# Optimization experiments

Hardware: AMD Instinct MI355X
Metric: run time of the kernel (lower is better)

Reference implementation:

```python
import jax, jax.numpy as jnp
import numpy as np

S_MAX = 512   # BERT max positions (module filters spans to <=512)


def setup_inputs() -> dict:
    key = jax.random.key(0)
    k1, k2, k3, k4, k5 = jax.random.split(key, 5)
    B, S, H = 8, 512, 768
    E, M, C = 16, 4, 96
    embedding = jax.random.normal(k1, (B, S, H), dtype=jnp.float32)
    # mean-over-heads last-layer attention rows (row-stochastic-ish positives)
    attention = jax.random.uniform(k2, (B, S, S), dtype=jnp.float32)
    attention = attention / attention.sum(-1, keepdims=True)
    mention_starts = jax.random.randint(k3, (B, E, M), 0, 500, dtype=jnp.int32)
    mention_lengths = jax.random.randint(k4, (B, E, M), 1, 6, dtype=jnp.int32)
    labels = jax.random.randint(k5, (B, E, E, C), 0, 2, dtype=jnp.int32)
    return {"embedding": embedding, "attention": attention,
            "mention_starts": mention_starts, "mention_lengths": mention_lengths,
            "labels": labels}


def reference(embedding, attention, mention_starts, mention_lengths, labels):
    # embedding: [B,S,H] BERT last_hidden_state
    # attention: [B,S,S] last-layer attention averaged over heads
    # mention spans (start, end): tokens start+1 .. end inclusive (per original slicing)
    B, S, H = embedding.shape
    E = mention_starts.shape[1]
    s_idx = jnp.arange(S, dtype=jnp.int32)
    ends = mention_starts + mention_lengths
    # token membership mask per entity: union over its mentions. [B,E,S]
    mask = ((s_idx >= (mention_starts + 1)[..., None]) &
            (s_idx <= ends[..., None])).any(axis=2)
    maskf = mask.astype(embedding.dtype)
    count = jnp.maximum(maskf.sum(-1, keepdims=True), 1.0)  # [B,E,1]
    # context[e] = mean over selected tokens t of attention[t] @ embedding
    att_rows = jnp.einsum('bes,bst->bet', maskf, attention)          # summed attention rows
    context = jnp.einsum('bet,bth->beh', att_rows, embedding) / count  # [B,E,H]
    # doc[e] = logsumexp over selected token embeddings (per hidden dim)
    masked = jnp.where(mask[..., None], embedding[:, None, :, :], -jnp.inf)  # [B,E,S,H]
    doc = jax.scipy.special.logsumexp(masked, axis=2)                # [B,E,H]
    cls = embedding[:, 0]                                            # [B,H]
    # all ordered entity pairs h != t (use_negative=True path)
    hh, tt = np.nonzero(~np.eye(E, dtype=bool))                      # static, P = E*(E-1)
    P = hh.shape[0]
    feat = jnp.stack([
        jnp.broadcast_to(cls[:, None, :], (B, P, H)),
        doc[:, hh],
        doc[:, tt],
        context[:, hh] * context[:, tt],
    ], axis=2)                                                       # [B,P,4,H]
    feature_set = feat.reshape(B * P, 4, H)
    labels_out = labels[:, hh, tt].reshape(B * P, -1)                # [B*P,C]
    return feature_set, labels_out
```

## Files before the change

### kernel.cpp

```cpp
#include <hip/hip_runtime.h>
#include <math.h>

#define Bc 8
#define Sc 512
#define Hc 768
#define Ec 16
#define Mc 4
#define Cc 96
#define Pc 240


__global__ __launch_bounds__(256) void k_mask_att_doc(
    const float* __restrict__ emb, const float* __restrict__ att,
    const int* __restrict__ starts, const int* __restrict__ lens,
    float* __restrict__ att_rows, float* __restrict__ cnt,
    float* __restrict__ docv, float* __restrict__ ctxu)
{
  int be = blockIdx.x;
  int b  = be >> 4;
  int tid = threadIdx.x;

  {
    float* z = ctxu + (size_t)be * Hc;
    z[tid] = 0.f; z[tid + 256] = 0.f; z[tid + 512] = 0.f;
  }

  __shared__ int slist[32];
  __shared__ int n_sh;
  if (tid == 0) n_sh = 0;
  __syncthreads();

  int base = be * Mc;
  int st0 = starts[base+0], st1 = starts[base+1];
  int st2 = starts[base+2], st3 = starts[base+3];
  int en0 = st0 + lens[base+0], en1 = st1 + lens[base+1];
  int en2 = st2 + lens[base+2], en3 = st3 + lens[base+3];

  for (int s = tid; s < Sc; s += 256) {
    bool in = (s > st0 && s <= en0) || (s > st1 && s <= en1) ||
              (s > st2 && s <= en2) || (s > st3 && s <= en3);
    if (in) { int pos = atomicAdd(&n_sh, 1); slist[pos] = s; }
  }
  __syncthreads();
  int n = n_sh;

  float2 a = make_float2(0.f, 0.f);
  for (int i = 0; i < n; ++i) {
    const float2* row2 =
        (const float2*)(att + ((size_t)b * Sc + slist[i]) * Sc);
    float2 v = row2[tid];
    a.x += v.x; a.y += v.y;
  }
  ((float2*)(att_rows + (size_t)be * Sc))[tid] = a;
  if (tid == 0) cnt[be] = (float)n;

  #pragma unroll
  for (int kk = 0; kk < 3; ++kk) {
    int h = tid + kk * 256;
    const float* ecol = emb + (size_t)b * Sc * Hc + h;
    float m = ecol[(size_t)slist[0] * Hc];
    float l = 1.0f;
    for (int i = 1; i < n; ++i) {
      float v  = ecol[(size_t)slist[i] * Hc];
      float nm = fmaxf(m, v);
      l = l * __expf(m - nm) + __expf(v - nm);
      m = nm;
    }
    docv[(size_t)be * Hc + h] = m + __logf(l);
  }
}

__global__ __launch_bounds__(256) void k_context(
    const float* __restrict__ emb, const float* __restrict__ att_rows,
    float* __restrict__ ctxu)
{
  int tchunk = blockIdx.x;
  int hchunk = blockIdx.y;
  int b      = blockIdx.z;
  int tid = threadIdx.x;
  int h  = hchunk * 256 + tid;
  int t0 = tchunk * 64;

  __shared__ float ar[64][20];
  {
    int e = tid >> 4, q = tid & 15;
    const float4* src =
        (const float4*)(att_rows + ((size_t)(b * Ec + e)) * Sc + t0);
    float4 v = src[q];
    ar[q*4+0][e] = v.x;
    ar[q*4+1][e] = v.y;
    ar[q*4+2][e] = v.z;
    ar[q*4+3][e] = v.w;
  }
  __syncthreads();

  float acc[16];
  #pragma unroll
  for (int e = 0; e < 16; ++e) acc[e] = 0.f;

  const float* ecol = emb + ((size_t)b * Sc + t0) * Hc + h;
  #pragma unroll 4
  for (int tt = 0; tt < 64; ++tt) {
    float ev = ecol[(size_t)tt * Hc];
    const float4* arv = (const float4*)&ar[tt][0];
    float4 a0 = arv[0], a1 = arv[1], a2 = arv[2], a3 = arv[3];
    acc[ 0] = fmaf(a0.x, ev, acc[ 0]);
    acc[ 1] = fmaf(a0.y, ev, acc[ 1]);
    acc[ 2] = fmaf(a0.z, ev, acc[ 2]);
    acc[ 3] = fmaf(a0.w, ev, acc[ 3]);
    acc[ 4] = fmaf(a1.x, ev, acc[ 4]);
    acc[ 5] = fmaf(a1.y, ev, acc[ 5]);
    acc[ 6] = fmaf(a1.z, ev, acc[ 6]);
    acc[ 7] = fmaf(a1.w, ev, acc[ 7]);
    acc[ 8] = fmaf(a2.x, ev, acc[ 8]);
    acc[ 9] = fmaf(a2.y, ev, acc[ 9]);
    acc[10] = fmaf(a2.z, ev, acc[10]);
    acc[11] = fmaf(a2.w, ev, acc[11]);
    acc[12] = fmaf(a3.x, ev, acc[12]);
    acc[13] = fmaf(a3.y, ev, acc[13]);
    acc[14] = fmaf(a3.z, ev, acc[14]);
    acc[15] = fmaf(a3.w, ev, acc[15]);
  }

  float* outb = ctxu + (size_t)(b * Ec) * Hc + h;
  #pragma unroll
  for (int e = 0; e < 16; ++e) atomicAdd(outb + (size_t)e * Hc, acc[e]);
}

__global__ __launch_bounds__(192) void k_assemble(
    const float* __restrict__ emb, const int* __restrict__ labels,
    const float* __restrict__ docv, const float* __restrict__ ctxu,
    const float* __restrict__ cnt, float* __restrict__ out)
{
  int r = blockIdx.x;
  int b = r / Pc, p = r % Pc;
  int i = p / 15, k = p % 15;
  int j = k + (k >= i ? 1 : 0);
  int tid = threadIdx.x;

  float ci = 1.0f / cnt[b * Ec + i];
  float cj = 1.0f / cnt[b * Ec + j];

  const float4* cls4 = (const float4*)(emb  + (size_t)b * Sc * Hc);
  const float4* di4  = (const float4*)(docv + (size_t)(b * Ec + i) * Hc);
  const float4* dj4  = (const float4*)(docv + (size_t)(b * Ec + j) * Hc);
  const float4* xi4  = (const float4*)(ctxu + (size_t)(b * Ec + i) * Hc);
  const float4* xj4  = (const float4*)(ctxu + (size_t)(b * Ec + j) * Hc);
  float4* o = (float4*)(out + (size_t)r * 4 * Hc);

  o[      tid] = cls4[tid];
  o[192 + tid] = di4[tid];
  o[384 + tid] = dj4[tid];
  float4 xa = xi4[tid], xb = xj4[tid], c;
  c.x = (xa.x * ci) * (xb.x * cj);
  c.y = (xa.y * ci) * (xb.y * cj);
  c.z = (xa.z * ci) * (xb.z * cj);
  c.w = (xa.w * ci) * (xb.w * cj);
  o[576 + tid] = c;

  if (tid < 24) {
    const int4* l4 =
        (const int4*)(labels + (((size_t)b * Ec + i) * Ec + j) * Cc);
    int4 v = l4[tid];
    float4 f;
    f.x = (float)v.x; f.y = (float)v.y; f.z = (float)v.z; f.w = (float)v.w;
    ((float4*)(out + (size_t)Bc * Pc * 4 * Hc + (size_t)r * Cc))[tid] = f;
  }
}

extern "C" void kernel_launch(void* const* d_in, const int* in_sizes, int n_in,
                              void* d_out, int out_size, void* d_ws, size_t ws_size,
                              hipStream_t stream) {
  const float* emb    = (const float*)d_in[0];
  const float* att    = (const float*)d_in[1];
  const int*   starts = (const int*)d_in[2];
  const int*   lens   = (const int*)d_in[3];
  const int*   labels = (const int*)d_in[4];
  float* out = (float*)d_out;

  float* att_rows = (float*)d_ws;
  float* cnt      = att_rows + (size_t)Bc * Ec * Sc;
  float* docv     = cnt      + (size_t)Bc * Ec;
  float* ctxu     = docv     + (size_t)Bc * Ec * Hc;

  k_mask_att_doc<<<Bc * Ec, 256, 0, stream>>>(emb, att, starts, lens,
                                              att_rows, cnt, docv, ctxu);
  k_context<<<dim3(8, 3, Bc), 256, 0, stream>>>(emb, att_rows, ctxu);
  k_assemble<<<Bc * Pc, 192, 0, stream>>>(emb, labels, docv, ctxu, cnt, out);
}
```

Measured before the change: 98.86 us.

## Fuse three kernels into one cooperative kernel with grid syncs

Merges the mask/attention/doc, context and assemble kernels into a single cooperatively launched kernel of 192 blocks, using grid-wide syncs between phases so that two kernel launches and their gaps go away. The logsumexp becomes a two-pass max-then-sum with four independent accumulators, and the attention-row gather is unrolled by four. Assembly now runs on only 192 blocks that each loop over 10 rows, which lowers parallelism for the output-write phase. Grid syncs add their own cost, and the two-pass logsumexp reads the gathered embeddings twice.

```diff
diff --git a/kernel.cpp b/kernel.cpp
--- a/kernel.cpp
+++ b/kernel.cpp
@@ -1,5 +1,8 @@
 #include <hip/hip_runtime.h>
+#include <hip/hip_cooperative_groups.h>
 #include <math.h>
+
+namespace cg = cooperative_groups;
 
 #define Bc 8
 #define Sc 512
@@ -8,163 +11,187 @@
 #define Mc 4
 #define Cc 96
 #define Pc 240
-
-
-__global__ __launch_bounds__(256) void k_mask_att_doc(
+#define NB 192
+
+
+__global__ __launch_bounds__(256) void k_fused(
     const float* __restrict__ emb, const float* __restrict__ att,
     const int* __restrict__ starts, const int* __restrict__ lens,
+    const int* __restrict__ labels,
     float* __restrict__ att_rows, float* __restrict__ cnt,
-    float* __restrict__ docv, float* __restrict__ ctxu)
+    float* __restrict__ docv, float* __restrict__ ctxu,
+    float* __restrict__ out)
 {
-  int be = blockIdx.x;
-  int b  = be >> 4;
-  int tid = threadIdx.x;
+  cg::grid_group gg = cg::this_grid();
+  const int bid = blockIdx.x;
+  const int tid = threadIdx.x;
+
+  __shared__ int   slist[32];
+  __shared__ int   n_sh;
+  __shared__ float ar[64][20];
+
+  if (bid < Bc * Ec) {
+    const int be = bid, b = be >> 4;
+
+    {
+      float* z = ctxu + (size_t)be * Hc;
+      z[tid] = 0.f; z[tid + 256] = 0.f; z[tid + 512] = 0.f;
+    }
+
+    if (tid == 0) n_sh = 0;
+    __syncthreads();
+    const int base = be * Mc;
+    const int st0 = starts[base+0], st1 = starts[base+1];
+    const int st2 = starts[base+2], st3 = starts[base+3];
+    const int en0 = st0 + lens[base+0], en1 = st1 + lens[base+1];
+    const int en2 = st2 + lens[base+2], en3 = st3 + lens[base+3];
+    for (int s = tid; s < Sc; s += 256) {
+      bool in = (s > st0 && s <= en0) || (s > st1 && s <= en1) ||
+                (s > st2 && s <= en2) || (s > st3 && s <= en3);
+      if (in) { int pos = atomicAdd(&n_sh, 1); slist[pos] = s; }
+    }
+    __syncthreads();
+    const int n = n_sh;
+
+    {
+      const float2* a2 = (const float2*)(att + (size_t)b * Sc * Sc);
+      float2 acc2 = make_float2(0.f, 0.f);
+      int i = 0;
+      for (; i + 4 <= n; i += 4) {
+        float2 v0 = a2[(size_t)slist[i+0] * (Sc/2) + tid];
+        float2 v1 = a2[(size_t)slist[i+1] * (Sc/2) + tid];
+        float2 v2 = a2[(size_t)slist[i+2] * (Sc/2) + tid];
+        float2 v3 = a2[(size_t)slist[i+3] * (Sc/2) + tid];
+        acc2.x += (v0.x + v1.x) + (v2.x + v3.x);
+        acc2.y += (v0.y + v1.y) + (v2.y + v3.y);
+      }
+      for (; i < n; ++i) {
+        float2 v = a2[(size_t)slist[i] * (Sc/2) + tid];
+        acc2.x += v.x; acc2.y += v.y;
+      }
+      ((float2*)(att_rows + (size_t)be * Sc))[tid] = acc2;
+      if (tid == 0) cnt[be] = (float)n;
+    }
+
+    #pragma unroll
+    for (int kk = 0; kk < 3; ++kk) {
+      const int h = tid + kk * 256;
+      const float* ecol = emb + (size_t)b * Sc * Hc + h;
+      float m0 = -3.4e38f, m1 = -3.4e38f, m2 = -3.4e38f, m3 = -3.4e38f;
+      int ii = 0;
+      for (; ii + 4 <= n; ii += 4) {
+        m0 = fmaxf(m0, ecol[(size_t)slist[ii+0] * Hc]);
+        m1 = fmaxf(m1, ecol[(size_t)slist[ii+1] * Hc]);
+        m2 = fmaxf(m2, ecol[(size_t)slist[ii+2] * Hc]);
+        m3 = fmaxf(m3, ecol[(size_t)slist[ii+3] * Hc]);
+      }
+      for (; ii < n; ++ii) m0 = fmaxf(m0, ecol[(size_t)slist[ii] * Hc]);
+      const float m = fmaxf(fmaxf(m0, m1), fmaxf(m2, m3));
+      float l0 = 0.f, l1 = 0.f, l2 = 0.f, l3 = 0.f;
+      ii = 0;
+      for (; ii + 4 <= n; ii += 4) {
+        l0 += __expf(ecol[(size_t)slist[ii+0] * Hc] - m);
+        l1 += __expf(ecol[(size_t)slist[ii+1] * Hc] - m);
+        l2 += __expf(ecol[(size_t)slist[ii+2] * Hc] - m);
+        l3 += __expf(ecol[(size_t)slist[ii+3] * Hc] - m);
+      }
+      for (; ii < n; ++ii) l0 += __expf(ecol[(size_t)slist[ii] * Hc] - m);
+      docv[(size_t)be * Hc + h] = m + __logf((l0 + l1) + (l2 + l3));
+    }
+  }
+
+  gg.sync();
 
   {
-    float* z = ctxu + (size_t)be * Hc;
-    z[tid] = 0.f; z[tid + 256] = 0.f; z[tid + 512] = 0.f;
+    const int tchunk = bid & 7;
+    const int hb     = bid >> 3;
+    const int hchunk = hb % 3;
+    const int b      = hb / 3;
+    const int h  = hchunk * 256 + tid;
+    const int t0 = tchunk * 64;
+
+    {
+      const int e = tid >> 4, q = tid & 15;
+      const float4* src =
+          (const float4*)(att_rows + ((size_t)(b * Ec + e)) * Sc + t0);
+      float4 v = src[q];
+      ar[q*4+0][e] = v.x;
+      ar[q*4+1][e] = v.y;
+      ar[q*4+2][e] = v.z;
+      ar[q*4+3][e] = v.w;
+    }
+    __syncthreads();
+
+    float acc[16];
+    #pragma unroll
+    for (int e = 0; e < 16; ++e) acc[e] = 0.f;
+
+    const float* ecol = emb + ((size_t)b * Sc + t0) * Hc + h;
+    #pragma unroll 8
+    for (int tt = 0; tt < 64; ++tt) {
+      float ev = ecol[(size_t)tt * Hc];
+      const float4* arv = (const float4*)&ar[tt][0];
+      float4 q0 = arv[0], q1 = arv[1], q2 = arv[2], q3 = arv[3];
+      acc[ 0] = fmaf(q0.x, ev, acc[ 0]);
+      acc[ 1] = fmaf(q0.y, ev, acc[ 1]);
+      acc[ 2] = fmaf(q0.z, ev, acc[ 2]);
+      acc[ 3] = fmaf(q0.w, ev, acc[ 3]);
+      acc[ 4] = fmaf(q1.x, ev, acc[ 4]);
+      acc[ 5] = fmaf(q1.y, ev, acc[ 5]);
+      acc[ 6] = fmaf(q1.z, ev, acc[ 6]);
+      acc[ 7] = fmaf(q1.w, ev, acc[ 7]);
+      acc[ 8] = fmaf(q2.x, ev, acc[ 8]);
+      acc[ 9] = fmaf(q2.y, ev, acc[ 9]);
+      acc[10] = fmaf(q2.z, ev, acc[10]);
+      acc[11] = fmaf(q2.w, ev, acc[11]);
+      acc[12] = fmaf(q3.x, ev, acc[12]);
+      acc[13] = fmaf(q3.y, ev, acc[13]);
+      acc[14] = fmaf(q3.z, ev, acc[14]);
+      acc[15] = fmaf(q3.w, ev, acc[15]);
+    }
+
+    float* outb = ctxu + (size_t)(b * Ec) * Hc + h;
+    #pragma unroll
+    for (int e = 0; e < 16; ++e) atomicAdd(outb + (size_t)e * Hc, acc[e]);
   }
 
-  __shared__ int slist[32];
-  __shared__ int n_sh;
-  if (tid == 0) n_sh = 0;
-  __syncthreads();
-
-  int base = be * Mc;
-  int st0 = starts[base+0], st1 = starts[base+1];
-  int st2 = starts[base+2], st3 = starts[base+3];
-  int en0 = st0 + lens[base+0], en1 = st1 + lens[base+1];
-  int en2 = st2 + lens[base+2], en3 = st3 + lens[base+3];
-
-  for (int s = tid; s < Sc; s += 256) {
-    bool in = (s > st0 && s <= en0) || (s > st1 && s <= en1) ||
-              (s > st2 && s <= en2) || (s > st3 && s <= en3);
-    if (in) { int pos = atomicAdd(&n_sh, 1); slist[pos] = s; }
-  }
-  __syncthreads();
-  int n = n_sh;
-
-  float2 a = make_float2(0.f, 0.f);
-  for (int i = 0; i < n; ++i) {
-    const float2* row2 =
-        (const float2*)(att + ((size_t)b * Sc + slist[i]) * Sc);
-    float2 v = row2[tid];
-    a.x += v.x; a.y += v.y;
-  }
-  ((float2*)(att_rows + (size_t)be * Sc))[tid] = a;
-  if (tid == 0) cnt[be] = (float)n;
-
-  #pragma unroll
-  for (int kk = 0; kk < 3; ++kk) {
-    int h = tid + kk * 256;
-    const float* ecol = emb + (size_t)b * Sc * Hc + h;
-    float m = ecol[(size_t)slist[0] * Hc];
-    float l = 1.0f;
-    for (int i = 1; i < n; ++i) {
-      float v  = ecol[(size_t)slist[i] * Hc];
-      float nm = fmaxf(m, v);
-      l = l * __expf(m - nm) + __expf(v - nm);
-      m = nm;
-    }
-    docv[(size_t)be * Hc + h] = m + __logf(l);
-  }
-}
-
-__global__ __launch_bounds__(256) void k_context(
-    const float* __restrict__ emb, const float* __restrict__ att_rows,
-    float* __restrict__ ctxu)
-{
-  int tchunk = blockIdx.x;
-  int hchunk = blockIdx.y;
-  int b      = blockIdx.z;
-  int tid = threadIdx.x;
-  int h  = hchunk * 256 + tid;
-  int t0 = tchunk * 64;
-
-  __shared__ float ar[64][20];
-  {
-    int e = tid >> 4, q = tid & 15;
-    const float4* src =
-        (const float4*)(att_rows + ((size_t)(b * Ec + e)) * Sc + t0);
-    float4 v = src[q];
-    ar[q*4+0][e] = v.x;
-    ar[q*4+1][e] = v.y;
-    ar[q*4+2][e] = v.z;
-    ar[q*4+3][e] = v.w;
-  }
-  __syncthreads();
-
-  float acc[16];
-  #pragma unroll
-  for (int e = 0; e < 16; ++e) acc[e] = 0.f;
-
-  const float* ecol = emb + ((size_t)b * Sc + t0) * Hc + h;
-  #pragma unroll 4
-  for (int tt = 0; tt < 64; ++tt) {
-    float ev = ecol[(size_t)tt * Hc];
-    const float4* arv = (const float4*)&ar[tt][0];
-    float4 a0 = arv[0], a1 = arv[1], a2 = arv[2], a3 = arv[3];
-    acc[ 0] = fmaf(a0.x, ev, acc[ 0]);
-    acc[ 1] = fmaf(a0.y, ev, acc[ 1]);
-    acc[ 2] = fmaf(a0.z, ev, acc[ 2]);
-    acc[ 3] = fmaf(a0.w, ev, acc[ 3]);
-    acc[ 4] = fmaf(a1.x, ev, acc[ 4]);
-    acc[ 5] = fmaf(a1.y, ev, acc[ 5]);
-    acc[ 6] = fmaf(a1.z, ev, acc[ 6]);
-    acc[ 7] = fmaf(a1.w, ev, acc[ 7]);
-    acc[ 8] = fmaf(a2.x, ev, acc[ 8]);
-    acc[ 9] = fmaf(a2.y, ev, acc[ 9]);
-    acc[10] = fmaf(a2.z, ev, acc[10]);
-    acc[11] = fmaf(a2.w, ev, acc[11]);
-    acc[12] = fmaf(a3.x, ev, acc[12]);
-    acc[13] = fmaf(a3.y, ev, acc[13]);
-    acc[14] = fmaf(a3.z, ev, acc[14]);
-    acc[15] = fmaf(a3.w, ev, acc[15]);
-  }
-
-  float* outb = ctxu + (size_t)(b * Ec) * Hc + h;
-  #pragma unroll
-  for (int e = 0; e < 16; ++e) atomicAdd(outb + (size_t)e * Hc, acc[e]);
-}
-
-__global__ __launch_bounds__(192) void k_assemble(
-    const float* __restrict__ emb, const int* __restrict__ labels,
-    const float* __restrict__ docv, const float* __restrict__ ctxu,
-    const float* __restrict__ cnt, float* __restrict__ out)
-{
-  int r = blockIdx.x;
-  int b = r / Pc, p = r % Pc;
-  int i = p / 15, k = p % 15;
-  int j = k + (k >= i ? 1 : 0);
-  int tid = threadIdx.x;
-
-  float ci = 1.0f / cnt[b * Ec + i];
-  float cj = 1.0f / cnt[b * Ec + j];
-
-  const float4* cls4 = (const float4*)(emb  + (size_t)b * Sc * Hc);
-  const float4* di4  = (const float4*)(docv + (size_t)(b * Ec + i) * Hc);
-  const float4* dj4  = (const float4*)(docv + (size_t)(b * Ec + j) * Hc);
-  const float4* xi4  = (const float4*)(ctxu + (size_t)(b * Ec + i) * Hc);
-  const float4* xj4  = (const float4*)(ctxu + (size_t)(b * Ec + j) * Hc);
-  float4* o = (float4*)(out + (size_t)r * 4 * Hc);
-
-  o[      tid] = cls4[tid];
-  o[192 + tid] = di4[tid];
-  o[384 + tid] = dj4[tid];
-  float4 xa = xi4[tid], xb = xj4[tid], c;
-  c.x = (xa.x * ci) * (xb.x * cj);
-  c.y = (xa.y * ci) * (xb.y * cj);
-  c.z = (xa.z * ci) * (xb.z * cj);
-  c.w = (xa.w * ci) * (xb.w * cj);
-  o[576 + tid] = c;
-
-  if (tid < 24) {
-    const int4* l4 =
-        (const int4*)(labels + (((size_t)b * Ec + i) * Ec + j) * Cc);
-    int4 v = l4[tid];
-    float4 f;
-    f.x = (float)v.x; f.y = (float)v.y; f.z = (float)v.z; f.w = (float)v.w;
-    ((float4*)(out + (size_t)Bc * Pc * 4 * Hc + (size_t)r * Cc))[tid] = f;
+  gg.sync();
+
+  const size_t lab_base = (size_t)Bc * Pc * 4 * Hc;
+  for (int rr = 0; rr < 10; ++rr) {
+    const int r = bid * 10 + rr;
+    const int b = r / Pc, p = r % Pc;
+    const int i = p / 15, kq = p % 15;
+    const int j = kq + (kq >= i ? 1 : 0);
+
+    const float4* cls4 = (const float4*)(emb  + (size_t)b * Sc * Hc);
+    const float4* di4  = (const float4*)(docv + (size_t)(b * Ec + i) * Hc);
+    const float4* dj4  = (const float4*)(docv + (size_t)(b * Ec + j) * Hc);
+    const float4* xi4  = (const float4*)(ctxu + (size_t)(b * Ec + i) * Hc);
+    const float4* xj4  = (const float4*)(ctxu + (size_t)(b * Ec + j) * Hc);
+    float4* o = (float4*)(out + (size_t)r * 4 * Hc);
+
+    if (tid < 192) {
+      const float ci = 1.0f / cnt[b * Ec + i];
+      const float cj = 1.0f / cnt[b * Ec + j];
+      o[      tid] = cls4[tid];
+      o[192 + tid] = di4[tid];
+      o[384 + tid] = dj4[tid];
+      float4 xa = xi4[tid], xb = xj4[tid], c;
+      c.x = (xa.x * ci) * (xb.x * cj);
+      c.y = (xa.y * ci) * (xb.y * cj);
+      c.z = (xa.z * ci) * (xb.z * cj);
+      c.w = (xa.w * ci) * (xb.w * cj);
+      o[576 + tid] = c;
+    } else if (tid < 216) {
+      const int q = tid - 192;
+      const int4* l4 =
+          (const int4*)(labels + (((size_t)b * Ec + i) * Ec + j) * Cc);
+      int4 v = l4[q];
+      float4 f;
+      f.x = (float)v.x; f.y = (float)v.y; f.z = (float)v.z; f.w = (float)v.w;
+      ((float4*)(out + lab_base + (size_t)r * Cc))[q] = f;
+    }
   }
 }
 
@@ -183,8 +210,10 @@
   float* docv     = cnt      + (size_t)Bc * Ec;
   float* ctxu     = docv     + (size_t)Bc * Ec * Hc;
 
-  k_mask_att_doc<<<Bc * Ec, 256, 0, stream>>>(emb, att, starts, lens,
-                                              att_rows, cnt, docv, ctxu);
-  k_context<<<dim3(8, 3, Bc), 256, 0, stream>>>(emb, att_rows, ctxu);
-  k_assemble<<<Bc * Pc, 192, 0, stream>>>(emb, labels, docv, ctxu, cnt, out);
+  void* args[] = {
+    (void*)&emb, (void*)&att, (void*)&starts, (void*)&lens, (void*)&labels,
+    (void*)&att_rows, (void*)&cnt, (void*)&docv, (void*)&ctxu, (void*)&out
+  };
+  hipLaunchCooperativeKernel((const void*)k_fused, dim3(NB), dim3(256),
+                             args, 0, stream);
 }
```

New measurement: 155.9 us. 57.7% more time.
